# Kernel optimization log

Measured on AMD Instinct MI355X. Metric: run time of the kernel, lower is better.

Reference implementation:

```python
import jax, jax.numpy as jnp
import numpy as np

# SLAYER neuron / simulation constants (from params)
THETA = 10.0      # spike threshold
TAU_SR = 10.0     # PSP (synaptic response) time constant
TS = 1.0          # simulation time step
TAU_RHO = 1.0     # surrogate-gradient width
SCALE_RHO = 1.0   # surrogate-gradient scale
ALPHA = float(np.exp(-TS / TAU_SR))  # leaky-filter decay per step

B, C_IN, T = 32, 156, 2048
HID, OUT = 512, 20


@jax.custom_vjp
def spike(u):
    # Hard threshold with SLAYER-style exponential surrogate gradient.
    return (u >= THETA).astype(u.dtype)

def _spike_fwd(u):
    return spike(u), u

def _spike_bwd(u, g):
    sg = (SCALE_RHO / TAU_RHO) * jnp.exp(-jnp.abs(u - THETA) / TAU_RHO)
    return (g * sg,)

spike.defvjp(_spike_fwd, _spike_bwd)


def psp(x):
    # Leaky exponential temporal filter along the LAST axis (SLAYER psp):
    # y[t] = ALPHA * y[t-1] + x[t]
    xt = jnp.moveaxis(x, -1, 0)  # [T, ...]
    def step(c, xi):
        c = ALPHA * c + xi
        return c, c
    _, y = jax.lax.scan(step, jnp.zeros_like(xt[0]), xt)
    return jnp.moveaxis(y, 0, -1)


def dense(x, W):
    # SLAYER dense layer: per-timestep fully-connected over channel dim.
    # x: [N, C, H, W, T], W: [O, C] -> [N, O, H, W, T]
    return jnp.einsum('oc,nchwt->nohwt', W, x)


def _make_perm():
    rng = np.random.default_rng(0)
    random_list = rng.permutation(np.arange(1, 40))
    perm = []
    for i in random_list:
        perm.append(2 * int(i) - 2)
        perm.append(2 * int(i) - 1)
    for i in random_list:
        perm.append(2 * int(i) - 2 + 78)
        perm.append(2 * int(i) - 1 + 78)
    return jnp.asarray(perm, dtype=jnp.int32)


def setup_inputs() -> dict:
    key = jax.random.key(0)
    k0, k1, k2, k3, k4 = jax.random.split(key, 5)
    spike_input = jax.random.randint(k0, (B, C_IN, 1, 1, T), 0, 2).astype(jnp.float32)
    W1 = jax.random.normal(k1, (HID, C_IN), dtype=jnp.float32) * (C_IN ** -0.5)
    W2 = jax.random.normal(k2, (OUT, HID), dtype=jnp.float32) * (HID ** -0.5)
    Wl1 = jax.random.normal(k3, (HID, T), dtype=jnp.float32) * (T ** -0.5)
    Wl2 = jax.random.normal(k4, (OUT, HID), dtype=jnp.float32) * (HID ** -0.5)
    perm = _make_perm()
    return {"spike_input": spike_input, "W1": W1, "W2": W2,
            "Wl1": Wl1, "Wl2": Wl2, "perm": perm}


def reference(spike_input, W1, W2, Wl1, Wl2, perm):
    # Branch 1: channel-dense over taxels, PSP + spike, twice.
    s1 = spike(psp(dense(spike_input, W1)))          # [B, HID, 1, 1, T]
    spike_output = spike(psp(dense(s1, W2)))         # [B, OUT, 1, 1, T]

    # Branch 2: transpose channel<->time, permute taxel axis, dense over time dim.
    x_t = jnp.swapaxes(spike_input, 1, 4)            # [B, T, 1, 1, C_IN]
    x_tp = x_t[..., perm]                            # gather on taxel axis
    l1 = spike(psp(dense(x_tp, Wl1)))                # [B, HID, 1, 1, C_IN]
    location_output = spike(psp(dense(l1, Wl2)))     # [B, OUT, 1, 1, C_IN]

    return jnp.concatenate([spike_output, location_output], axis=4)
```

## Files before the change

kernel.cpp:

```cpp
#include <hip/hip_runtime.h>

#define ALPHA  0.90483741803595952f
#define ALPHA8 0.44932896411722156f
#define A64C   5.82e-23f
#define THETA  10.0f
#define BF1    ((unsigned short)0x3F80)
#define ISCALE 0.015625f

typedef short   bf16x8 __attribute__((ext_vector_type(8)));
typedef float   f32x4  __attribute__((ext_vector_type(4)));
typedef float   f32x4v __attribute__((ext_vector_type(4)));
typedef unsigned short ushort4v __attribute__((ext_vector_type(4)));
typedef unsigned short ushort8v __attribute__((ext_vector_type(8)));
typedef unsigned char  uchar4v  __attribute__((ext_vector_type(4)));
typedef unsigned char  uchar8v  __attribute__((ext_vector_type(8)));
typedef long long i64;

#define DMA16(gsrc, ldst)                                                     \
    __builtin_amdgcn_global_load_lds(                                         \
        (const __attribute__((address_space(1))) unsigned int*)(gsrc),        \
        (__attribute__((address_space(3))) unsigned int*)(ldst), 16, 0, 0)

__device__ __forceinline__ unsigned short f2bf(float f) {
    unsigned int x = __float_as_uint(f);
    unsigned int r = (x + 0x7FFFu + ((x >> 16) & 1u)) >> 16;
    return (unsigned short)r;
}
__device__ __forceinline__ float bf2f(unsigned short h) {
    return __uint_as_float(((unsigned int)h) << 16);
}
__device__ __forceinline__ void split2(float w, unsigned short& h0,
                                       unsigned short& h1) {
    h0 = f2bf(w);          float r0 = w - bf2f(h0);
    h1 = f2bf(r0);
}
__device__ __forceinline__ unsigned char f2fp8(float f) {
    int pk = __builtin_amdgcn_cvt_pk_fp8_f32(f, 0.f, 0, false);
    return (unsigned char)(pk & 0xFF);
}
__device__ __forceinline__ float fp82f(unsigned char b) {
    return __builtin_amdgcn_cvt_f32_fp8((int)b, 0);
}

__global__ __launch_bounds__(256) void prep_scan_pack(
    const float* __restrict__ In, unsigned char* __restrict__ Infp8,
    unsigned short* __restrict__ Pbf,
    const float* __restrict__ W1,  const float* __restrict__ W2,
    const float* __restrict__ Wl1, const float* __restrict__ Wl2,
    unsigned short* __restrict__ W1p,  unsigned char* __restrict__ W2p8,
    unsigned char* __restrict__ Wl1p8, unsigned short* __restrict__ Wl2p)
{
    const int blk = blockIdx.x;
    const int tid = threadIdx.x;
    if (blk < 1088) {
        if (blk < 512) {
            int m = blk;
            for (int k = tid; k < 2048; k += 256) {
                float w = Wl1[(long long)m * 2048 + k] * 64.0f;
                unsigned char h0 = f2fp8(w);
                unsigned char h1 = f2fp8(w - fp82f(h0));
                Wl1p8[(long long)m * 2048 + k] = h0;
                Wl1p8[1048576 + (long long)m * 2048 + k] = h1;
            }
        } else if (blk < 1024) {
            int m = blk - 512;
            for (int k = tid; k < 160; k += 256) {
                float v = (k < 156) ? W1[(long long)m * 156 + k] : 0.f;
                unsigned short h0, h1;
                split2(v, h0, h1);
                W1p[(long long)m * 160 + k] = h0;
                W1p[81920 + (long long)m * 160 + k] = h1;
            }
        } else if (blk < 1056) {
            int m = blk - 1024;
            for (int k = tid; k < 512; k += 256) {
                float w = (m < 20) ? W2[(long long)m * 512 + k] : 0.f;
                unsigned char h0 = f2fp8(w);
                unsigned char h1 = f2fp8(w - fp82f(h0));
                W2p8[(long long)m * 512 + k] = h0;
                W2p8[16384 + (long long)m * 512 + k] = h1;
            }
        } else {
            int m = blk - 1056;
            for (int k = tid; k < 512; k += 256) {
                float v = (m < 20) ? Wl2[(long long)m * 512 + k] : 0.f;
                unsigned short h0, h1;
                split2(v, h0, h1);
                Wl2p[(long long)m * 512 + k] = h0;
                Wl2p[16384 + (long long)m * 512 + k] = h1;
            }
        }
        return;
    }

    const int row = blk - 1088;
    const float* x = In + (long long)row * 2048 + tid * 8;
    const unsigned char ONE8 = f2fp8(1.0f);

    float v[8];
    *(f32x4v*)&v[0] = *(const f32x4v*)x;
    *(f32x4v*)&v[4] = *(const f32x4v*)(x + 4);

    uchar8v raw;
    #pragma unroll
    for (int k = 0; k < 8; ++k) raw[k] = (v[k] >= 0.5f) ? ONE8 : (unsigned char)0;
    *(uchar8v*)(Infp8 + (long long)row * 2048 + tid * 8) = raw;

    float y = 0.f;
    #pragma unroll
    for (int k = 0; k < 8; ++k) { y = ALPHA * y + v[k]; v[k] = y; }

    const int lane = tid & 63, wid = tid >> 6;
    float val = y, mm = ALPHA8;
    #pragma unroll
    for (int d = 1; d < 64; d <<= 1) {
        float p = __shfl_up(val, d);
        if (lane >= d) val += mm * p;
        mm *= mm;
    }
    __shared__ float wsum[4];
    if (lane == 63) wsum[wid] = val;
    __syncthreads();
    float pw = 0.f;
    #pragma unroll
    for (int w2 = 0; w2 < 3; ++w2)
        if (w2 < wid) pw = pw * A64C + wsum[w2];
    float prev = __shfl_up(val, 1);
    float a8l  = __expf(-0.8f * (float)lane);
    float carry = (lane == 0) ? pw : (prev + a8l * pw);

    ushort8v pv;
    float ak = ALPHA;
    #pragma unroll
    for (int k = 0; k < 8; ++k) {
        float yk = v[k] + ak * carry;
        ak *= ALPHA;
        pv[k] = f2bf(yk);
    }
    *(ushort8v*)(Pbf + (long long)row * 2048 + tid * 8) = pv;
}

__global__ __launch_bounds__(256) void transposeP(
    const unsigned short* __restrict__ Pbf, unsigned short* __restrict__ PT)
{
    __shared__ unsigned short Tile[64][72];
    const int t0 = blockIdx.x * 64;
    const int c0 = blockIdx.y * 64;
    const int b  = blockIdx.z;
    const int tid = threadIdx.x;

    #pragma unroll
    for (int s = 0; s < 2; ++s) {
        int id = tid + s * 256;
        int cc = id >> 3;
        int t8 = (id & 7) * 8;
        ushort8v v = {0,0,0,0,0,0,0,0};
        if (c0 + cc < 156)
            v = *(const ushort8v*)(Pbf + (long long)(b * 156 + c0 + cc) * 2048 + t0 + t8);
        int chunk = ((t8 >> 3) ^ (cc >> 3)) & 7;
        *(ushort8v*)&Tile[cc][chunk * 8] = v;
    }
    __syncthreads();

    #pragma unroll
    for (int s = 0; s < 2; ++s) {
        int id = tid + s * 256;
        int t  = id >> 3;
        int c8 = (id & 7) * 8;
        if (c0 + c8 + 7 < 160) {
            unsigned short r[8];
            #pragma unroll
            for (int j = 0; j < 8; ++j) {
                int col = ((((t >> 3) ^ ((c8 + j) >> 3)) & 7) << 3) | (t & 7);
                r[j] = Tile[c8 + j][col];
            }
            *(ushort8v*)(PT + (long long)b * 327680 + (long long)(t0 + t) * 160 + c0 + c8)
                = *(ushort8v*)r;
        }
    }
}

__global__ __launch_bounds__(256) void mega_gemm1(
    const unsigned short* __restrict__ W1p,
    const unsigned short* __restrict__ PT,
    unsigned short* __restrict__ S1bits,
    const unsigned char* __restrict__ Wl1p8,
    const unsigned char* __restrict__ Infp8,
    unsigned short* __restrict__ Zp)
{
    __shared__ alignas(16) unsigned char SMEM[49152];
    const int bx  = blockIdx.x;
    const int tid = threadIdx.x;
    const int lane = tid & 63, w = tid >> 6;
    const int wy = w >> 1, wx = w & 1;
    const int l15 = lane & 15, kq = lane >> 4;
    const int key = (l15 >> 1) & 3;

    if (bx >= 1280) {
        unsigned char* Ab = SMEM;
        unsigned char* Bb = SMEM + 32768;

        const int id1 = bx - 1280;
        const int z  = id1 >> 6;
        const int m0 = ((id1 >> 4) & 3) * 128;
        const int n0 = (id1 & 15) * 128;
        const unsigned short* Tb = PT + (long long)z * 327680;

        const unsigned short* gA[4]; int ldsA[4];
        #pragma unroll
        for (int s = 0; s < 4; ++s) {
            int id = tid + s * 256;
            int pl = id >> 9, m = (id >> 2) & 127, g = id & 3;
            int gs = g ^ ((m >> 1) & 3);
            gA[s] = W1p + (long long)pl * 81920 + (long long)(m0 + m) * 160 + gs * 8;
            ldsA[s] = id * 16;
        }
        const unsigned short* gB[2]; int ldsB[2];
        #pragma unroll
        for (int s = 0; s < 2; ++s) {
            int id = tid + s * 256;
            int n = id >> 2, g = id & 3;
            int gs = g ^ ((n >> 1) & 3);
            gB[s] = Tb + (long long)(n0 + n) * 160 + gs * 8;
            ldsB[s] = id * 16;
        }

        auto dmaA = [&](int buf) {
            unsigned char* dst = Ab + buf * 16384;
            #pragma unroll
            for (int s = 0; s < 4; ++s) { DMA16(gA[s], dst + ldsA[s]); gA[s] += 32; }
        };
        auto dmaB = [&](int buf) {
            unsigned char* dst = Bb + buf * 8192;
            #pragma unroll
            for (int s = 0; s < 2; ++s) { DMA16(gB[s], dst + ldsB[s]); gB[s] += 32; }
        };

        int aOff[2][4], bOff[4];
        #pragma unroll
        for (int pl = 0; pl < 2; ++pl)
            #pragma unroll
            for (int mt = 0; mt < 4; ++mt)
                aOff[pl][mt] = pl * 8192 + (wy * 64 + mt * 16 + l15) * 64 +
                               ((kq ^ key) * 16);
        #pragma unroll
        for (int nt = 0; nt < 4; ++nt)
            bOff[nt] = (wx * 64 + nt * 16 + l15) * 64 + ((kq ^ key) * 16);

        f32x4 acc[4][4] = {};

        dmaA(0); dmaB(0);
        __syncthreads();

        #pragma unroll
        for (int it = 0; it < 5; ++it) {
            const int cur = it & 1;
            if (it < 4) { dmaA(cur ^ 1); dmaB(cur ^ 1); }

            const unsigned char* Ac = Ab + cur * 16384;
            const unsigned char* Bc = Bb + cur * 8192;
            bf16x8 bfr[4];
            #pragma unroll
            for (int nt = 0; nt < 4; ++nt)
                bfr[nt] = *(const bf16x8*)(Bc + bOff[nt]);
            #pragma unroll
            for (int pl = 0; pl < 2; ++pl) {
                #pragma unroll
                for (int mt = 0; mt < 4; ++mt) {
                    bf16x8 afr = *(const bf16x8*)(Ac + aOff[pl][mt]);
                    #pragma unroll
                    for (int nt = 0; nt < 4; ++nt)
                        acc[mt][nt] = __builtin_amdgcn_mfma_f32_16x16x32_bf16(
                            afr, bfr[nt], acc[mt][nt], 0, 0, 0);
                }
            }
            __syncthreads();
        }

        unsigned short* Db = S1bits + (long long)z * 512 * 128;
        #pragma unroll
        for (int mt = 0; mt < 4; ++mt) {
            #pragma unroll
            for (int i = 0; i < 4; ++i) {
                int m = m0 + wy * 64 + mt * 16 + kq * 4 + i;
                #pragma unroll
                for (int nt = 0; nt < 4; ++nt) {
                    unsigned long long mask = __ballot(acc[mt][nt][i] >= THETA);
                    if (l15 == 0) {
                        int nchunk = (n0 + wx * 64 + nt * 16) >> 4;
                        Db[(long long)nchunk * 512 + m] =
                            (unsigned short)((mask >> (kq * 16)) & 0xFFFFu);
                    }
                }
            }
        }
    } else {
        unsigned char* Ab = SMEM;
        unsigned char* Bb = SMEM + 16384;

        const int id0 = bx;
        const int nIdx = id0 % 40;
        if (nIdx >= 39) return;
        const int rest = id0 / 40;
        const int n0  = nIdx * 128;
        const int m0  = (rest & 7) * 64;
        const int ksl = rest >> 3;
        const int ks0 = ksl * 512;

        const unsigned char* gA8[2]; int ldsA8[2];
        #pragma unroll
        for (int s = 0; s < 2; ++s) {
            int id = tid + s * 256;
            int pl = id >> 8, m = (id >> 2) & 63, g = id & 3;
            int gs = g ^ ((m >> 1) & 3);
            gA8[s] = Wl1p8 + (long long)pl * 1048576 +
                     (long long)(m0 + m) * 2048 + ks0 + gs * 16;
            ldsA8[s] = id * 16;
        }
        const unsigned char* gB8[2]; int ldsB8[2];
        #pragma unroll
        for (int s = 0; s < 2; ++s) {
            int id = tid + s * 256;
            int n = id >> 2, g = id & 3;
            int gs = g ^ ((n >> 1) & 3);
            gB8[s] = Infp8 + (long long)(n0 + n) * 2048 + ks0 + gs * 16;
            ldsB8[s] = id * 16;
        }

        auto dmaA8 = [&](int buf) {
            unsigned char* dst = Ab + buf * 8192;
            #pragma unroll
            for (int s = 0; s < 2; ++s) { DMA16(gA8[s], dst + ldsA8[s]); gA8[s] += 64; }
        };
        auto dmaB8 = [&](int buf) {
            unsigned char* dst = Bb + buf * 8192;
            #pragma unroll
            for (int s = 0; s < 2; ++s) { DMA16(gB8[s], dst + ldsB8[s]); gB8[s] += 64; }
        };

        int aO8[2][2][2], bO8[4][2];
        #pragma unroll
        for (int ks = 0; ks < 2; ++ks) {
            const int gl = ks * 2 + (kq >> 1);
            const int sub = ((gl ^ key) * 16) + (kq & 1) * 8;
            #pragma unroll
            for (int pl = 0; pl < 2; ++pl)
                #pragma unroll
                for (int mt = 0; mt < 2; ++mt)
                    aO8[pl][mt][ks] = pl * 4096 +
                        (wy * 32 + mt * 16 + l15) * 64 + sub;
            #pragma unroll
            for (int nt = 0; nt < 4; ++nt)
                bO8[nt][ks] = (wx * 64 + nt * 16 + l15) * 64 + sub;
        }

        f32x4 acc[2][4] = {};

        dmaA8(0); dmaB8(0);
        __syncthreads();

        #pragma unroll
        for (int it = 0; it < 8; ++it) {
            const int cur = it & 1;
            if (it < 7) { dmaA8(cur ^ 1); dmaB8(cur ^ 1); }

            const unsigned char* Ac = Ab + cur * 8192;
            const unsigned char* Bc = Bb + cur * 8192;
            #pragma unroll
            for (int ks = 0; ks < 2; ++ks) {
                i64 bfr[4];
                #pragma unroll
                for (int nt = 0; nt < 4; ++nt)
                    bfr[nt] = *(const i64*)(Bc + bO8[nt][ks]);
                #pragma unroll
                for (int pl = 0; pl < 2; ++pl) {
                    #pragma unroll
                    for (int mt = 0; mt < 2; ++mt) {
                        i64 afr = *(const i64*)(Ac + aO8[pl][mt][ks]);
                        #pragma unroll
                        for (int nt = 0; nt < 4; ++nt)
                            acc[mt][nt] = __builtin_amdgcn_mfma_f32_16x16x32_fp8_fp8(
                                afr, bfr[nt], acc[mt][nt], 0, 0, 0);
                    }
                }
            }
            __syncthreads();
        }

        unsigned short* Tu = (unsigned short*)SMEM;
        #pragma unroll
        for (int mt = 0; mt < 2; ++mt) {
            #pragma unroll
            for (int i = 0; i < 4; ++i) {
                int mL = wy * 32 + mt * 16 + kq * 4 + i;
                #pragma unroll
                for (int nt = 0; nt < 4; ++nt) {
                    int nL = wx * 64 + nt * 16 + l15;
                    Tu[mL * 130 + nL] = f2bf(acc[mt][nt][i] * ISCALE);
                }
            }
        }
        __syncthreads();

        unsigned short* Zs = Zp + (long long)ksl * 2555904;
        #pragma unroll
        for (int s2 = 0; s2 < 32; ++s2) {
            int id = tid + s2 * 256;
            int cL = id >> 6;
            int mL = id & 63;
            int n = n0 + cL;
            int bb = n / 156, cc = n - bb * 156;
            Zs[(long long)cc * 16384 + bb * 512 + m0 + mL] = Tu[mL * 130 + cL];
        }
    }
}

__global__ __launch_bounds__(256) void mega_stage2(
    const unsigned char* __restrict__ W2p8,
    const unsigned short* __restrict__ S1bits,
    float* __restrict__ C2p,
    const unsigned short* __restrict__ Zp,
    const int* __restrict__ perm,
    unsigned short* __restrict__ L1T)
{
    __shared__ alignas(16) unsigned char SMEM[27648];
    const int bx  = blockIdx.x;
    const int tid = threadIdx.x;

    if (bx >= 512) {
        auto As = (unsigned char (*)[2][32][72])SMEM;
        auto Bs = (unsigned char (*)[128][72])(SMEM + 9216);

        const int bxg = bx - 512;
        const int lane = tid & 63, w = tid >> 6;
        const int l15 = lane & 15, kq = lane >> 4;
        const int n0  = (bxg & 15) * 128;
        const int b   = bxg >> 4;

        const unsigned short* Bb = S1bits + (long long)b * 512 * 128;
        const unsigned char ONE8 = f2fp8(1.0f);

        int aPl[2], aM[2], aK8[2];
        #pragma unroll
        for (int s = 0; s < 2; ++s) {
            int id = tid + s * 256;
            aPl[s] = id >> 8; int rem = id & 255;
            aM[s] = rem >> 3; aK8[s] = (rem & 7) * 8;
        }
        const int kb = (tid >> 4) * 4;
        const int nb = (tid & 15) * 8;
        const int nchunk = (n0 + nb) >> 4;
        const int nshift = nb & 15;

        f32x4 acc[2][2] = {};
        uchar8v aReg[2];
        unsigned short bBits[4];

        auto loadA = [&](int k0) {
            #pragma unroll
            for (int s = 0; s < 2; ++s)
                aReg[s] = *(const uchar8v*)(W2p8 + (long long)aPl[s] * 16384 +
                                            (long long)aM[s] * 512 + k0 + aK8[s]);
        };
        auto loadB = [&](int k0) {
            unsigned long long u = *(const unsigned long long*)
                (Bb + (long long)nchunk * 512 + k0 + kb);
            bBits[0] = (unsigned short)u;
            bBits[1] = (unsigned short)(u >> 16);
            bBits[2] = (unsigned short)(u >> 32);
            bBits[3] = (unsigned short)(u >> 48);
        };
        auto stage = [&](int buf) {
            #pragma unroll
            for (int s = 0; s < 2; ++s) *(uchar8v*)&As[buf][aPl[s]][aM[s]][aK8[s]] = aReg[s];
            unsigned char bv[4][8];
            #pragma unroll
            for (int kk2 = 0; kk2 < 4; ++kk2) {
                unsigned int bits = ((unsigned int)bBits[kk2] >> nshift) & 0xFFu;
                #pragma unroll
                for (int j = 0; j < 8; ++j)
                    bv[kk2][j] = ((bits >> j) & 1u) ? ONE8 : (unsigned char)0;
            }
            #pragma unroll
            for (int j = 0; j < 8; ++j) {
                uchar4v v4 = { bv[0][j], bv[1][j], bv[2][j], bv[3][j] };
                *(uchar4v*)&Bs[buf][nb + j][kb] = v4;
            }
        };

        loadA(0); loadB(0);
        stage(0);
        __syncthreads();

        #pragma unroll
        for (int it = 0; it < 8; ++it) {
            const int cur = it & 1;
            const int kn = (it + 1) * 64;
            if (it < 7) { loadA(kn); loadB(kn); }

            #pragma unroll
            for (int ks = 0; ks < 2; ++ks) {
                i64 bfr[2];
                #pragma unroll
                for (int nt = 0; nt < 2; ++nt)
                    bfr[nt] = *(const i64*)&Bs[cur][w * 32 + nt * 16 + l15][ks * 32 + kq * 8];
                #pragma unroll
                for (int pl = 0; pl < 2; ++pl) {
                    #pragma unroll
                    for (int mt = 0; mt < 2; ++mt) {
                        i64 afr = *(const i64*)&As[cur][pl][mt * 16 + l15][ks * 32 + kq * 8];
                        #pragma unroll
                        for (int nt = 0; nt < 2; ++nt)
                            acc[mt][nt] = __builtin_amdgcn_mfma_f32_16x16x32_fp8_fp8(
                                afr, bfr[nt], acc[mt][nt], 0, 0, 0);
                    }
                }
            }

            if (it < 7) stage(cur ^ 1);
            __syncthreads();
        }

        float* Cb = C2p + (long long)b * 20 * 2048;
        #pragma unroll
        for (int mt = 0; mt < 2; ++mt) {
            #pragma unroll
            for (int i = 0; i < 4; ++i) {
                int m = mt * 16 + kq * 4 + i;
                if (m >= 20) continue;
                #pragma unroll
                for (int nt = 0; nt < 2; ++nt) {
                    int n = n0 + w * 32 + nt * 16 + l15;
                    Cb[(long long)m * 2048 + n] = acc[mt][nt][i];
                }
            }
        }
    } else {
        auto Xs = (float (*)[32])SMEM;
        int* p  = (int*)(SMEM + 19968);

        const int r0 = bx * 32;
        for (int i = tid; i < 156; i += 256) p[i] = perm[i];

        const int row = tid & 31;
        const int cq  = tid >> 5;
        #pragma unroll
        for (int it = 0; it < 20; ++it) {
            int c = it * 8 + cq;
            if (c < 156) {
                long long base = (long long)c * 16384 + r0 + row;
                float s = bf2f(Zp[base]) + bf2f(Zp[base + 2555904]) +
                          bf2f(Zp[base + 2 * 2555904]) + bf2f(Zp[base + 3 * 2555904]);
                Xs[c][row] = s;
            }
        }
        __syncthreads();

        if (tid < 32) {
            float y = 0.f;
            for (int c = 0; c < 156; ++c) {
                y = ALPHA * y + Xs[p[c]][tid];
                L1T[(long long)c * 16384 + r0 + tid] = (y >= THETA) ? BF1 : 0;
            }
        }
    }
}

__global__ __launch_bounds__(256) void mega_stage3(
    const float* __restrict__ C2p, float* __restrict__ out,
    const unsigned short* __restrict__ Wl2p,
    const unsigned short* __restrict__ L1T)
{
    __shared__ alignas(16) unsigned char SMEM[36864];
    const int bx  = blockIdx.x;
    const int tid = threadIdx.x;

    if (bx >= 32) {
        const int row = bx - 32;
        const float* x = C2p + (long long)row * 2048 + tid * 8;

        float v[8];
        *(f32x4v*)&v[0] = *(const f32x4v*)x;
        *(f32x4v*)&v[4] = *(const f32x4v*)(x + 4);

        float y = 0.f;
        #pragma unroll
        for (int k = 0; k < 8; ++k) { y = ALPHA * y + v[k]; v[k] = y; }

        const int lane = tid & 63, wid = tid >> 6;
        float val = y, mm = ALPHA8;
        #pragma unroll
        for (int d = 1; d < 64; d <<= 1) {
            float p = __shfl_up(val, d);
            if (lane >= d) val += mm * p;
            mm *= mm;
        }
        float* wsum = (float*)SMEM;
        if (lane == 63) wsum[wid] = val;
        __syncthreads();
        float pw = 0.f;
        #pragma unroll
        for (int w2 = 0; w2 < 3; ++w2)
            if (w2 < wid) pw = pw * A64C + wsum[w2];
        float prev = __shfl_up(val, 1);
        float a8l  = __expf(-0.8f * (float)lane);
        float carry = (lane == 0) ? pw : (prev + a8l * pw);

        float* o = out + (long long)row * 2204 + tid * 8;
        float ak = ALPHA;
        #pragma unroll
        for (int k = 0; k < 8; ++k) {
            float yk = v[k] + ak * carry;
            ak *= ALPHA;
            o[k] = (yk >= THETA) ? 1.0f : 0.0f;
        }
    } else {
        auto As = (unsigned short (*)[32][72])SMEM;
        auto Bs = (unsigned short (*)[72])(SMEM + 9216);

        const int b  = bx;
        const int lane = tid & 63, w = tid >> 6;
        const int l15 = lane & 15, kq = lane >> 4;

        f32x4 acc[2][3] = {};

        for (int k0 = 0; k0 < 512; k0 += 64) {
            #pragma unroll
            for (int s = 0; s < 2; ++s) {
                int id = tid + s * 256;
                int pl = id >> 8, rem = id & 255;
                int m = rem >> 3, k8 = (rem & 7) * 8;
                ushort8v v = *(const ushort8v*)(Wl2p + (long long)pl * 16384 +
                                                (long long)m * 512 + k0 + k8);
                *(ushort8v*)&As[pl][m][k8] = v;
            }
            #pragma unroll
            for (int s = 0; s < 6; ++s) {
                int id = tid + s * 256;
                int n = id >> 3, k8 = (id & 7) * 8;
                ushort8v v = {0,0,0,0,0,0,0,0};
                if (n < 156)
                    v = *(const ushort8v*)(L1T + (long long)n * 16384 +
                                           b * 512 + k0 + k8);
                *(ushort8v*)&Bs[n][k8] = v;
            }
            __syncthreads();

            #pragma unroll
            for (int ks = 0; ks < 2; ++ks) {
                bf16x8 bfr[3];
                #pragma unroll
                for (int nt = 0; nt < 3; ++nt)
                    bfr[nt] = *(const bf16x8*)&Bs[w * 48 + nt * 16 + l15][ks * 32 + kq * 8];
                #pragma unroll
                for (int s = 0; s < 2; ++s) {
                    #pragma unroll
                    for (int mt = 0; mt < 2; ++mt) {
                        bf16x8 afr = *(const bf16x8*)&As[s][mt * 16 + l15][ks * 32 + kq * 8];
                        #pragma unroll
                        for (int nt = 0; nt < 3; ++nt)
                            acc[mt][nt] = __builtin_amdgcn_mfma_f32_16x16x32_bf16(
                                afr, bfr[nt], acc[mt][nt], 0, 0, 0);
                    }
                }
            }
            __syncthreads();
        }

        float* Cs = (float*)SMEM;
        #pragma unroll
        for (int mt = 0; mt < 2; ++mt) {
            #pragma unroll
            for (int i = 0; i < 4; ++i) {
                int m = mt * 16 + kq * 4 + i;
                #pragma unroll
                for (int nt = 0; nt < 3; ++nt) {
                    int n = w * 48 + nt * 16 + l15;
                    Cs[m * 193 + n] = acc[mt][nt][i];
                }
            }
        }
        __syncthreads();

        if (tid < 20) {
            const float* cr = Cs + tid * 193;
            float* o = out + (long long)(b * 20 + tid) * 2204 + 2048;
            float y = 0.f;
            for (int c = 0; c < 156; ++c) {
                y = ALPHA * y + cr[c];
                o[c] = (y >= THETA) ? 1.0f : 0.0f;
            }
        }
    }
}

extern "C" void kernel_launch(void* const* d_in, const int* in_sizes, int n_in,
                              void* d_out, int out_size, void* d_ws, size_t ws_size,
                              hipStream_t stream)
{
    const float* In  = (const float*)d_in[0];
    const float* W1  = (const float*)d_in[1];
    const float* W2  = (const float*)d_in[2];
    const float* Wl1 = (const float*)d_in[3];
    const float* Wl2 = (const float*)d_in[4];
    const int*  perm = (const int*)d_in[5];
    float* out = (float*)d_out;

    float* ws = (float*)d_ws;
    unsigned short* S1bits = (unsigned short*)ws;
    float* C2p = ws + 1048576LL;
    unsigned char*  Infp8 = (unsigned char*)(ws + 3670016LL);
    unsigned short* Pbf  = (unsigned short*)(ws + 6225920LL);
    unsigned short* PT   = (unsigned short*)(ws + 11337728LL);
    unsigned short* W1p  = (unsigned short*)(ws + 16580608LL);
    unsigned char*  W2p8 = (unsigned char*)(ws + 16662528LL);
    unsigned char*  Wl1p8= (unsigned char*)(ws + 16670720LL);
    unsigned short* Wl2p = (unsigned short*)(ws + 17195008LL);
    unsigned short* Zpbf = (unsigned short*)(ws + 17211392LL);
    unsigned short* L1T  = (unsigned short*)(ws + 22323200LL);

    dim3 blk(256);

    prep_scan_pack<<<dim3(6080), blk, 0, stream>>>(
        In, Infp8, Pbf, W1, W2, Wl1, Wl2, W1p, W2p8, Wl1p8, Wl2p);
    transposeP<<<dim3(32, 3, 32), blk, 0, stream>>>(Pbf, PT);

    mega_gemm1<<<dim3(3328), blk, 0, stream>>>(W1p, PT, S1bits,
                                               Wl1p8, Infp8, Zpbf);
    mega_stage2<<<dim3(1024), blk, 0, stream>>>(W2p8, S1bits, C2p,
                                                Zpbf, perm, L1T);
    mega_stage3<<<dim3(672), blk, 0, stream>>>(C2p, out, Wl2p, L1T);

    (void)in_sizes; (void)n_in; (void)out_size; (void)ws_size;
}
```

Measured before the change: 176.4 us.

## Drop transpose kernel and read PSP tiles via LDS transpose loads

```diff
diff --git a/kernel.cpp b/kernel.cpp
--- a/kernel.cpp
+++ b/kernel.cpp
@@ -20,6 +20,14 @@
     __builtin_amdgcn_global_load_lds(                                         \
         (const __attribute__((address_space(1))) unsigned int*)(gsrc),        \
         (__attribute__((address_space(3))) unsigned int*)(ldst), 16, 0, 0)
+
+__device__ __forceinline__ i64 tr16(const unsigned char* p) {
+    i64 r;
+    asm volatile("ds_read_b64_tr_b16 %0, %1"
+                 : "=v"(r)
+                 : "v"((const __attribute__((address_space(3))) unsigned char*)p));
+    return r;
+}
 
 __device__ __forceinline__ unsigned short f2bf(float f) {
     unsigned int x = __float_as_uint(f);
@@ -52,6 +60,13 @@
 {
     const int blk = blockIdx.x;
     const int tid = threadIdx.x;
+    if (blk >= 6080) {
+        int idx = blk - 6080;
+        int b = idx >> 2, c = 156 + (idx & 3);
+        ushort8v z = {0,0,0,0,0,0,0,0};
+        *(ushort8v*)(Pbf + (long long)(b * 160 + c) * 2048 + tid * 8) = z;
+        return;
+    }
     if (blk < 1088) {
         if (blk < 512) {
             int m = blk;
@@ -94,6 +109,8 @@
     }
 
     const int row = blk - 1088;
+    const int bN  = row / 156;
+    const int prow = bN * 160 + (row - bN * 156);
     const float* x = In + (long long)row * 2048 + tid * 8;
     const unsigned char ONE8 = f2fp8(1.0f);
 
@@ -137,52 +154,12 @@
         ak *= ALPHA;
         pv[k] = f2bf(yk);
     }
-    *(ushort8v*)(Pbf + (long long)row * 2048 + tid * 8) = pv;
-}
-
-__global__ __launch_bounds__(256) void transposeP(
-    const unsigned short* __restrict__ Pbf, unsigned short* __restrict__ PT)
-{
-    __shared__ unsigned short Tile[64][72];
-    const int t0 = blockIdx.x * 64;
-    const int c0 = blockIdx.y * 64;
-    const int b  = blockIdx.z;
-    const int tid = threadIdx.x;
-
-    #pragma unroll
-    for (int s = 0; s < 2; ++s) {
-        int id = tid + s * 256;
-        int cc = id >> 3;
-        int t8 = (id & 7) * 8;
-        ushort8v v = {0,0,0,0,0,0,0,0};
-        if (c0 + cc < 156)
-            v = *(const ushort8v*)(Pbf + (long long)(b * 156 + c0 + cc) * 2048 + t0 + t8);
-        int chunk = ((t8 >> 3) ^ (cc >> 3)) & 7;
-        *(ushort8v*)&Tile[cc][chunk * 8] = v;
-    }
-    __syncthreads();
-
-    #pragma unroll
-    for (int s = 0; s < 2; ++s) {
-        int id = tid + s * 256;
-        int t  = id >> 3;
-        int c8 = (id & 7) * 8;
-        if (c0 + c8 + 7 < 160) {
-            unsigned short r[8];
-            #pragma unroll
-            for (int j = 0; j < 8; ++j) {
-                int col = ((((t >> 3) ^ ((c8 + j) >> 3)) & 7) << 3) | (t & 7);
-                r[j] = Tile[c8 + j][col];
-            }
-            *(ushort8v*)(PT + (long long)b * 327680 + (long long)(t0 + t) * 160 + c0 + c8)
-                = *(ushort8v*)r;
-        }
-    }
+    *(ushort8v*)(Pbf + (long long)prow * 2048 + tid * 8) = pv;
 }
 
 __global__ __launch_bounds__(256) void mega_gemm1(
     const unsigned short* __restrict__ W1p,
-    const unsigned short* __restrict__ PT,
+    const unsigned short* __restrict__ Pbf,
     unsigned short* __restrict__ S1bits,
     const unsigned char* __restrict__ Wl1p8,
     const unsigned char* __restrict__ Infp8,
@@ -204,7 +181,6 @@
         const int z  = id1 >> 6;
         const int m0 = ((id1 >> 4) & 3) * 128;
         const int n0 = (id1 & 15) * 128;
-        const unsigned short* Tb = PT + (long long)z * 327680;
 
         const unsigned short* gA[4]; int ldsA[4];
         #pragma unroll
@@ -215,14 +191,13 @@
             gA[s] = W1p + (long long)pl * 81920 + (long long)(m0 + m) * 160 + gs * 8;
             ldsA[s] = id * 16;
         }
-        const unsigned short* gB[2]; int ldsB[2];
+        const unsigned short* gB[2];
         #pragma unroll
         for (int s = 0; s < 2; ++s) {
             int id = tid + s * 256;
-            int n = id >> 2, g = id & 3;
-            int gs = g ^ ((n >> 1) & 3);
-            gB[s] = Tb + (long long)(n0 + n) * 160 + gs * 8;
-            ldsB[s] = id * 16;
+            int c  = ((id >> 6) << 2) | ((id >> 1) & 3);
+            int t8 = ((((id >> 3) & 7) << 1) | (id & 1)) << 3;
+            gB[s] = Pbf + (long long)(z * 160 + c) * 2048 + n0 + t8;
         }
 
         auto dmaA = [&](int buf) {
@@ -233,19 +208,20 @@
         auto dmaB = [&](int buf) {
             unsigned char* dst = Bb + buf * 8192;
             #pragma unroll
-            for (int s = 0; s < 2; ++s) { DMA16(gB[s], dst + ldsB[s]); gB[s] += 32; }
+            for (int s = 0; s < 2; ++s) {
+                DMA16(gB[s], dst + (tid + s * 256) * 16);
+                gB[s] += 65536;
+            }
         };
 
-        int aOff[2][4], bOff[4];
+        int aOff[2][4];
         #pragma unroll
         for (int pl = 0; pl < 2; ++pl)
             #pragma unroll
             for (int mt = 0; mt < 4; ++mt)
                 aOff[pl][mt] = pl * 8192 + (wy * 64 + mt * 16 + l15) * 64 +
                                ((kq ^ key) * 16);
-        #pragma unroll
-        for (int nt = 0; nt < 4; ++nt)
-            bOff[nt] = (wx * 64 + nt * 16 + l15) * 64 + ((kq ^ key) * 16);
+        const int bTr = wx * 512 + kq * 1920;
 
         f32x4 acc[4][4] = {};
 
@@ -258,11 +234,18 @@
             if (it < 4) { dmaA(cur ^ 1); dmaB(cur ^ 1); }
 
             const unsigned char* Ac = Ab + cur * 16384;
-            const unsigned char* Bc = Bb + cur * 8192;
+            const unsigned char* vB = Bb + cur * 8192 + bTr;
             bf16x8 bfr[4];
             #pragma unroll
-            for (int nt = 0; nt < 4; ++nt)
-                bfr[nt] = *(const bf16x8*)(Bc + bOff[nt]);
+            for (int nt = 0; nt < 4; ++nt) {
+                union { i64 q[2]; bf16x8 v; } u;
+                u.q[0] = tr16(vB + nt * 128);
+                u.q[1] = tr16(vB + 1024 + nt * 128);
+                bfr[nt] = u.v;
+            }
+            asm volatile("s_waitcnt lgkmcnt(0)" ::: "memory");
+            __builtin_amdgcn_sched_barrier(0);
+
             #pragma unroll
             for (int pl = 0; pl < 2; ++pl) {
                 #pragma unroll
@@ -711,7 +694,6 @@
     float* C2p = ws + 1048576LL;
     unsigned char*  Infp8 = (unsigned char*)(ws + 3670016LL);
     unsigned short* Pbf  = (unsigned short*)(ws + 6225920LL);
-    unsigned short* PT   = (unsigned short*)(ws + 11337728LL);
     unsigned short* W1p  = (unsigned short*)(ws + 16580608LL);
     unsigned char*  W2p8 = (unsigned char*)(ws + 16662528LL);
     unsigned char*  Wl1p8= (unsigned char*)(ws + 16670720LL);
@@ -721,11 +703,10 @@
 
     dim3 blk(256);
 
-    prep_scan_pack<<<dim3(6080), blk, 0, stream>>>(
+    prep_scan_pack<<<dim3(6208), blk, 0, stream>>>(
         In, Infp8, Pbf, W1, W2, Wl1, Wl2, W1p, W2p8, Wl1p8, Wl2p);
-    transposeP<<<dim3(32, 3, 32), blk, 0, stream>>>(Pbf, PT);
-
-    mega_gemm1<<<dim3(3328), blk, 0, stream>>>(W1p, PT, S1bits,
+
+    mega_gemm1<<<dim3(3328), blk, 0, stream>>>(W1p, Pbf, S1bits,
                                                Wl1p8, Infp8, Zpbf);
     mega_stage2<<<dim3(1024), blk, 0, stream>>>(W2p8, S1bits, C2p,
                                                 Zpbf, perm, L1T);
```

Result: no change. 176.5 us (+0.1%).
